# Kernel tuning notes

Hardware: AMD Instinct MI355X
Metric: run time of the kernel (lower is better)

## Reference

```python
import jax, jax.numpy as jnp
import numpy as np

POOL = (2, 2)
STRIDES = (2, 2)


def setup_inputs() -> dict:
    key = jax.random.key(0)
    k1, k2 = jax.random.split(key)
    B, H, W, C = 32, 64, 64, 128
    oH, oW = H * STRIDES[0], W * STRIDES[1]  # SAME padding
    updates = jax.random.normal(k1, (B, H, W, C), dtype=jnp.float32)
    mask = jax.random.randint(k2, (B, H, W, C), 0, oH * oW * C, dtype=jnp.int32)
    return {"updates": updates, "mask": mask}


def reference(updates, mask):
    B, H, W, C = updates.shape
    oH, oW, oC = H * STRIDES[0], W * STRIDES[1], C  # SAME padding output shape
    m = mask.astype(jnp.int32)
    # Decode flat per-batch index into (y, x); feature/batch come from position.
    y = m // (oW * oC)                      # [B,H,W,C]
    x = (m // oC) % oW                      # [B,H,W,C]
    b = jnp.arange(B, dtype=jnp.int32)[:, None, None, None]  # broadcasts over H,W,C
    f = jnp.arange(oC, dtype=jnp.int32)                      # broadcasts over last dim
    out = jnp.zeros((B, oH, oW, oC), dtype=updates.dtype)
    # tf.scatter_nd sums duplicate indices -> use .add for identical semantics
    return out.at[b, y, x, f].add(updates)
```

## Files before the change

### kernel.cpp

```cpp
#include <hip/hip_runtime.h>


#define HWC (64 * 64 * 128)
#define QBINS 4096

__global__ __launch_bounds__(256, 2) void unpool_q4(
    const float* __restrict__ upd, const int* __restrict__ mask,
    float* __restrict__ out)
{
    __shared__ float acc[QBINS * 4];

    int bid = blockIdx.x;
    int b   = bid & 31;
    int c0  = (bid >> 5) << 2;

    int t = threadIdx.x;

    const float4* ub = (const float4*)(upd  + (size_t)b * HWC + c0);
    const int4*   mb = (const int4*)  (mask + (size_t)b * HWC + c0);
    float*        ob = out + ((size_t)b << 21) + c0;

    float4 u[16];
    int4   m[16];
    #pragma unroll
    for (int k = 0; k < 16; ++k) {
        int pos = t + k * 256;
        u[k] = ub[pos * 32];
        m[k] = mb[pos * 32];
    }

    float4* a4 = (float4*)acc;

    for (int q = 0; q < 4; ++q) {
        #pragma unroll
        for (int k = 0; k < 16; ++k)
            a4[t + k * 256] = make_float4(0.f, 0.f, 0.f, 0.f);
        __syncthreads();

        #pragma unroll
        for (int k = 0; k < 16; ++k) {
            int b0 = m[k].x >> 7; if ((b0 >> 12) == q) atomicAdd(&acc[((b0 & 4095) << 2) + 0], u[k].x);
            int b1 = m[k].y >> 7; if ((b1 >> 12) == q) atomicAdd(&acc[((b1 & 4095) << 2) + 1], u[k].y);
            int b2 = m[k].z >> 7; if ((b2 >> 12) == q) atomicAdd(&acc[((b2 & 4095) << 2) + 2], u[k].z);
            int b3 = m[k].w >> 7; if ((b3 >> 12) == q) atomicAdd(&acc[((b3 & 4095) << 2) + 3], u[k].w);
        }
        __syncthreads();

        #pragma unroll
        for (int k = 0; k < 16; ++k) {
            int p = t + k * 256;
            float4 v = a4[p];
            *(float4*)(ob + (size_t)(q * QBINS + p) * 128) = v;
        }
        if (q < 3) __syncthreads();
    }
}

extern "C" void kernel_launch(void* const* d_in, const int* in_sizes, int n_in,
                              void* d_out, int out_size, void* d_ws, size_t ws_size,
                              hipStream_t stream) {
    const float* upd  = (const float*)d_in[0];
    const int*   mask = (const int*)d_in[1];
    float*       out  = (float*)d_out;

    unpool_q4<<<1024, 256, 0, stream>>>(upd, mask, out);
}
```

Before: 454.2 us.

## Halve LDS bins with eight passes and pack mask indices to 16 bits

Shrinks the per-block shared accumulator from 64KB to 32KB by splitting the output pixel range into eight passes instead of four, and raises launch bounds to four blocks per CU. Mask indices are pre-shifted and packed two per 32-bit register to cut register use. The aim is higher occupancy to hide global-load and atomic latency. The cost is twice as many barrier/zero/flush rounds and twice as many predicate scans over the held elements.

```diff
diff --git a/kernel.cpp b/kernel.cpp
--- a/kernel.cpp
+++ b/kernel.cpp
@@ -2,13 +2,14 @@
 
 
 #define HWC (64 * 64 * 128)
-#define QBINS 4096
+#define PBINS 2048
+#define NPASS 8
 
-__global__ __launch_bounds__(256, 2) void unpool_q4(
+__global__ __launch_bounds__(256, 4) void unpool_p8(
     const float* __restrict__ upd, const int* __restrict__ mask,
     float* __restrict__ out)
 {
-    __shared__ float acc[QBINS * 4];
+    __shared__ float acc[PBINS * 4];
 
     int bid = blockIdx.x;
     int b   = bid & 31;
@@ -21,38 +22,49 @@
     float*        ob = out + ((size_t)b << 21) + c0;
 
     float4 u[16];
-    int4   m[16];
+    uint2  pk[16];
     #pragma unroll
     for (int k = 0; k < 16; ++k) {
         int pos = t + k * 256;
         u[k] = ub[pos * 32];
-        m[k] = mb[pos * 32];
+        int4 m4 = mb[pos * 32];
+        unsigned b0 = ((unsigned)m4.x) >> 7;
+        unsigned b1 = ((unsigned)m4.y) >> 7;
+        unsigned b2 = ((unsigned)m4.z) >> 7;
+        unsigned b3 = ((unsigned)m4.w) >> 7;
+        pk[k].x = b0 | (b1 << 16);
+        pk[k].y = b2 | (b3 << 16);
     }
 
     float4* a4 = (float4*)acc;
 
-    for (int q = 0; q < 4; ++q) {
+    for (int q = 0; q < NPASS; ++q) {
         #pragma unroll
-        for (int k = 0; k < 16; ++k)
+        for (int k = 0; k < 8; ++k)
             a4[t + k * 256] = make_float4(0.f, 0.f, 0.f, 0.f);
         __syncthreads();
 
+        unsigned uq = (unsigned)q;
         #pragma unroll
         for (int k = 0; k < 16; ++k) {
-            int b0 = m[k].x >> 7; if ((b0 >> 12) == q) atomicAdd(&acc[((b0 & 4095) << 2) + 0], u[k].x);
-            int b1 = m[k].y >> 7; if ((b1 >> 12) == q) atomicAdd(&acc[((b1 & 4095) << 2) + 1], u[k].y);
-            int b2 = m[k].z >> 7; if ((b2 >> 12) == q) atomicAdd(&acc[((b2 & 4095) << 2) + 2], u[k].z);
-            int b3 = m[k].w >> 7; if ((b3 >> 12) == q) atomicAdd(&acc[((b3 & 4095) << 2) + 3], u[k].w);
+            unsigned b0 = pk[k].x & 0xffffu;
+            unsigned b1 = pk[k].x >> 16;
+            unsigned b2 = pk[k].y & 0xffffu;
+            unsigned b3 = pk[k].y >> 16;
+            if ((b0 >> 11) == uq) atomicAdd(&acc[((b0 & 2047u) << 2) + 0], u[k].x);
+            if ((b1 >> 11) == uq) atomicAdd(&acc[((b1 & 2047u) << 2) + 1], u[k].y);
+            if ((b2 >> 11) == uq) atomicAdd(&acc[((b2 & 2047u) << 2) + 2], u[k].z);
+            if ((b3 >> 11) == uq) atomicAdd(&acc[((b3 & 2047u) << 2) + 3], u[k].w);
         }
         __syncthreads();
 
         #pragma unroll
-        for (int k = 0; k < 16; ++k) {
+        for (int k = 0; k < 8; ++k) {
             int p = t + k * 256;
             float4 v = a4[p];
-            *(float4*)(ob + (size_t)(q * QBINS + p) * 128) = v;
+            *(float4*)(ob + (size_t)(q * PBINS + p) * 128) = v;
         }
-        if (q < 3) __syncthreads();
+        if (q < NPASS - 1) __syncthreads();
     }
 }
 
@@ -63,5 +75,5 @@
     const int*   mask = (const int*)d_in[1];
     float*       out  = (float*)d_out;
 
-    unpool_q4<<<1024, 256, 0, stream>>>(upd, mask, out);
+    unpool_p8<<<1024, 256, 0, stream>>>(upd, mask, out);
 }
```

Result: slower. 866.9 us (+90.9%).

## Use full-bin LDS histogram per two-channel block instead of four-pass quartering

Applied to the files above, without the earlier changes.

Each block now owns two channels of one batch and keeps all 16384 output bins in a 128KB dynamic LDS buffer, so the scatter happens in a single pass with no quarter filtering or repeated rescans. The grid grows to 2048 blocks of 1024 threads, with a swizzled block-to-(batch, channel-group) mapping. The aim is to remove the four passes of predicated atomics and the extra syncs. The trade-offs are narrower 8-byte global loads and stores across a 512-byte stride and at most one block per CU, because of the large LDS allocation.

```diff
diff --git a/kernel.cpp b/kernel.cpp
--- a/kernel.cpp
+++ b/kernel.cpp
@@ -1,58 +1,51 @@
 #include <hip/hip_runtime.h>
 
 
-#define HWC (64 * 64 * 128)
-#define QBINS 4096
+#define HWC   (64 * 64 * 128)
+#define NBINS 16384
 
-__global__ __launch_bounds__(256, 2) void unpool_q4(
+__global__ __launch_bounds__(1024) void unpool_fp2(
     const float* __restrict__ upd, const int* __restrict__ mask,
     float* __restrict__ out)
 {
-    __shared__ float acc[QBINS * 4];
+    extern __shared__ float acc[];
 
     int bid = blockIdx.x;
-    int b   = bid & 31;
-    int c0  = (bid >> 5) << 2;
+    int x   = bid & 7;
+    int r   = bid >> 3;
+    int g   = x * 8 + (r & 7);
+    int b   = r >> 3;
+    int c0  = g << 1;
 
     int t = threadIdx.x;
 
-    const float4* ub = (const float4*)(upd  + (size_t)b * HWC + c0);
-    const int4*   mb = (const int4*)  (mask + (size_t)b * HWC + c0);
-    float*        ob = out + ((size_t)b << 21) + c0;
+    const float* ubase = upd  + (size_t)b * HWC + c0;
+    const int*   mbase = mask + (size_t)b * HWC + c0;
+    float*       obase = out + ((size_t)b << 21) + c0;
 
-    float4 u[16];
-    int4   m[16];
+    float4* a4 = (float4*)acc;
+    #pragma unroll
+    for (int k = 0; k < 8; ++k)
+        a4[t + k * 1024] = make_float4(0.f, 0.f, 0.f, 0.f);
+    __syncthreads();
+
+    #pragma unroll
+    for (int k = 0; k < 4; ++k) {
+        int pos = t + (k << 10);
+        float2 u2 = *(const float2*)(ubase + (size_t)pos * 128);
+        int2   m2 = *(const int2*)  (mbase + (size_t)pos * 128);
+        unsigned b0 = ((unsigned)m2.x) >> 7;
+        unsigned b1 = ((unsigned)m2.y) >> 7;
+        atomicAdd(&acc[(b0 << 1) + 0], u2.x);
+        atomicAdd(&acc[(b1 << 1) + 1], u2.y);
+    }
+    __syncthreads();
+
     #pragma unroll
     for (int k = 0; k < 16; ++k) {
-        int pos = t + k * 256;
-        u[k] = ub[pos * 32];
-        m[k] = mb[pos * 32];
-    }
-
-    float4* a4 = (float4*)acc;
-
-    for (int q = 0; q < 4; ++q) {
-        #pragma unroll
-        for (int k = 0; k < 16; ++k)
-            a4[t + k * 256] = make_float4(0.f, 0.f, 0.f, 0.f);
-        __syncthreads();
-
-        #pragma unroll
-        for (int k = 0; k < 16; ++k) {
-            int b0 = m[k].x >> 7; if ((b0 >> 12) == q) atomicAdd(&acc[((b0 & 4095) << 2) + 0], u[k].x);
-            int b1 = m[k].y >> 7; if ((b1 >> 12) == q) atomicAdd(&acc[((b1 & 4095) << 2) + 1], u[k].y);
-            int b2 = m[k].z >> 7; if ((b2 >> 12) == q) atomicAdd(&acc[((b2 & 4095) << 2) + 2], u[k].z);
-            int b3 = m[k].w >> 7; if ((b3 >> 12) == q) atomicAdd(&acc[((b3 & 4095) << 2) + 3], u[k].w);
-        }
-        __syncthreads();
-
-        #pragma unroll
-        for (int k = 0; k < 16; ++k) {
-            int p = t + k * 256;
-            float4 v = a4[p];
-            *(float4*)(ob + (size_t)(q * QBINS + p) * 128) = v;
-        }
-        if (q < 3) __syncthreads();
+        int bin = t + (k << 10);
+        float2 v = *(const float2*)(acc + (bin << 1));
+        *(float2*)(obase + (size_t)bin * 128) = v;
     }
 }
 
@@ -63,5 +56,9 @@
     const int*   mask = (const int*)d_in[1];
     float*       out  = (float*)d_out;
 
-    unpool_q4<<<1024, 256, 0, stream>>>(upd, mask, out);
+    hipFuncSetAttribute((const void*)unpool_fp2,
+                        hipFuncAttributeMaxDynamicSharedMemorySize,
+                        NBINS * 2 * 4);
+
+    unpool_fp2<<<2048, 1024, NBINS * 2 * 4, stream>>>(upd, mask, out);
 }
```

Measured after the change: 586.4 us. +29.1%, slower.
